# Kernel optimization log

Hardware: AMD Instinct MI355X
Metric: run time of the kernel (lower is better)

## Reference

```python
import jax, jax.numpy as jnp
import numpy as np

SIZE = 1024
N_HEAD = 16
HEAD_DIM = SIZE // N_HEAD


def setup_inputs() -> dict:
    key = jax.random.key(0)
    ks = jax.random.split(key, 5)
    s = 1.0 / np.sqrt(SIZE)
    return {
        "x": jax.random.normal(ks[0], (4, 2048, SIZE), dtype=jnp.float32),
        "w_qkv": jax.random.uniform(ks[1], (SIZE, 3 * SIZE), dtype=jnp.float32, minval=-s, maxval=s),
        "b_qkv": jax.random.uniform(ks[2], (3 * SIZE,), dtype=jnp.float32, minval=-s, maxval=s),
        "w_fc": jax.random.uniform(ks[3], (SIZE, SIZE), dtype=jnp.float32, minval=-s, maxval=s),
        "b_fc": jax.random.uniform(ks[4], (SIZE,), dtype=jnp.float32, minval=-s, maxval=s),
    }


def reference(x, w_qkv, b_qkv, w_fc, b_fc):
    B, S, D = x.shape
    qkv = x @ w_qkv + b_qkv                      # [B, S, 3D]
    qkv = qkv.reshape(B, S, 3, N_HEAD, HEAD_DIM)
    qkv = jnp.transpose(qkv, (2, 0, 3, 1, 4))    # [3, B, H, S, hd]
    q, k, v = qkv[0], qkv[1], qkv[2]
    scale = 1.0 / np.sqrt(HEAD_DIM).astype(np.float32)
    scores = jnp.einsum('bhqd,bhkd->bhqk', q, k) * scale
    attn = jax.nn.softmax(scores, axis=-1)
    out = jnp.einsum('bhqk,bhkd->bhqd', attn, v)  # [B, H, S, hd]
    out = jnp.transpose(out, (0, 2, 1, 3)).reshape(B, S, D)
    return out @ w_fc + b_fc
```

## Files before the change

kernel.cpp:

```cpp
#include <hip/hip_runtime.h>

#define DEV __device__ __forceinline__

typedef float  f32x4  __attribute__((ext_vector_type(4)));
typedef short  short8 __attribute__((ext_vector_type(8)));
typedef __bf16 bf16x8 __attribute__((ext_vector_type(8)));

DEV f32x4 mfma_bf16(short8 a, short8 b, f32x4 c) {
    return __builtin_amdgcn_mfma_f32_16x16x32_bf16(
        __builtin_bit_cast(bf16x8, a), __builtin_bit_cast(bf16x8, b), c, 0, 0, 0);
}

DEV void gload_lds16(const void* g, void* l) {
    __builtin_amdgcn_global_load_lds(
        (const __attribute__((address_space(1))) unsigned int*)g,
        (__attribute__((address_space(3))) unsigned int*)l, 16, 0, 0);
}

DEV short f2bf(float f) {
    return __builtin_bit_cast(short, (__bf16)f);
}

__global__ void cast_x(const float* __restrict__ in, unsigned short* __restrict__ out, int n) {
    int i = (blockIdx.x * 256 + threadIdx.x) * 8;
    if (i >= n) return;
    f32x4 a = *(const f32x4*)(in + i);
    f32x4 b = *(const f32x4*)(in + i + 4);
    short8 o;
    o[0] = f2bf(a[0]); o[1] = f2bf(a[1]); o[2] = f2bf(a[2]); o[3] = f2bf(a[3]);
    o[4] = f2bf(b[0]); o[5] = f2bf(b[1]); o[6] = f2bf(b[2]); o[7] = f2bf(b[3]);
    *(short8*)(out + i) = o;
}

__global__ void transpose_cast(const float* __restrict__ in, unsigned short* __restrict__ out,
                               int R, int C) {
    __shared__ float tile[64][65];
    int c0 = blockIdx.x * 64, r0 = blockIdx.y * 64;
    int tx = threadIdx.x & 63, ty = threadIdx.x >> 6;
#pragma unroll
    for (int i = 0; i < 16; i++) {
        int r = i * 4 + ty;
        tile[r][tx] = in[(size_t)(r0 + r) * C + c0 + tx];
    }
    __syncthreads();
#pragma unroll
    for (int i = 0; i < 16; i++) {
        int cc = i * 4 + ty;
        out[(size_t)(c0 + cc) * R + r0 + tx] = (unsigned short)f2bf(tile[tx][cc]);
    }
}

__global__ void transpose_v(const unsigned short* __restrict__ Vb,
                            unsigned short* __restrict__ Vt) {
    __shared__ __align__(16) unsigned short tile[64][72];
    const int t = threadIdx.x;
    const int s0 = blockIdx.x * 64;
    const size_t slab = (size_t)blockIdx.y * 2048 * 64;
#pragma unroll
    for (int i = 0; i < 2; i++) {
        int c = i * 256 + t;
        int s = c >> 3, ch = c & 7;
        short8 v = *(const short8*)(Vb + slab + (size_t)(s0 + s) * 64 + ch * 8);
        *(short8*)(&tile[s][ch * 8]) = v;
    }
    __syncthreads();
#pragma unroll
    for (int i = 0; i < 2; i++) {
        int c = i * 256 + t;
        int d = c & 63, sc = c >> 6;
        short8 o;
#pragma unroll
        for (int e = 0; e < 8; e++) o[e] = tile[sc * 8 + e][d];
        *(short8*)(Vt + slab + (size_t)d * 2048 + s0 + sc * 8) = o;
    }
}

template <int MODE>
__global__ __launch_bounds__(256, 2) void gemm_bt(
    const unsigned short* __restrict__ A, const unsigned short* __restrict__ Bt,
    const float* __restrict__ bias, float* __restrict__ out_f32,
    unsigned short* __restrict__ q_out, unsigned short* __restrict__ k_out,
    unsigned short* __restrict__ v_out, int K) {
    __shared__ __align__(16) char smem[32768];
    char* lA = smem;
    char* lB = smem + 16384;
    const int t = threadIdx.x;
    const int lane = t & 63, w = t >> 6;
    const int wr = w >> 1, wc = w & 1;
    const int rowBase = blockIdx.y * 128, colBase = blockIdx.x * 128;

    f32x4 acc[4][4] = {};

    for (int k0 = 0; k0 < K; k0 += 64) {
#pragma unroll
        for (int i = 0; i < 4; i++) {
            int c = i * 256 + t;
            int r = c >> 3, j = c & 7;
            int jj = j ^ (r & 7);
            gload_lds16(A  + (size_t)(rowBase + r) * K + k0 + jj * 8, lA + c * 16);
            gload_lds16(Bt + (size_t)(colBase + r) * K + k0 + jj * 8, lB + c * 16);
        }
        __syncthreads();
#pragma unroll
        for (int ks = 0; ks < 2; ks++) {
            const int colb = (ks * 4 + (lane >> 4)) * 16;
            short8 af[4], bfr[4];
#pragma unroll
            for (int m2 = 0; m2 < 4; m2++) {
                int r = wr * 64 + m2 * 16 + (lane & 15);
                af[m2] = *(const short8*)(lA + r * 128 + (colb ^ ((r & 7) << 4)));
            }
#pragma unroll
            for (int n2 = 0; n2 < 4; n2++) {
                int r = wc * 64 + n2 * 16 + (lane & 15);
                bfr[n2] = *(const short8*)(lB + r * 128 + (colb ^ ((r & 7) << 4)));
            }
#pragma unroll
            for (int m2 = 0; m2 < 4; m2++)
#pragma unroll
                for (int n2 = 0; n2 < 4; n2++)
                    acc[m2][n2] = mfma_bf16(af[m2], bfr[n2], acc[m2][n2]);
        }
        __syncthreads();
    }

#pragma unroll
    for (int n2 = 0; n2 < 4; n2++) {
        int gc = colBase + wc * 64 + n2 * 16 + (lane & 15);
        float bv = bias[gc];
#pragma unroll
        for (int m2 = 0; m2 < 4; m2++) {
            int grb = rowBase + wr * 64 + m2 * 16 + ((lane >> 4) << 2);
#pragma unroll
            for (int r2 = 0; r2 < 4; r2++) {
                int gr = grb + r2;
                float v = acc[m2][n2][r2] + bv;
                if (MODE == 0) {
                    int which = gc >> 10, rem = gc & 1023;
                    int h = rem >> 6, d = rem & 63;
                    int b = gr >> 11, s = gr & 2047;
                    size_t idx = ((size_t)((b * 16 + h) * 2048 + s)) * 64 + d;
                    unsigned short* dst = which == 0 ? q_out : (which == 1 ? k_out : v_out);
                    if (which == 0) v *= 0.18033688011112042f;
                    dst[idx] = (unsigned short)f2bf(v);
                } else {
                    out_f32[(size_t)gr * 1024 + gc] = v;
                }
            }
        }
    }
}

__global__ __launch_bounds__(256, 4) void fattn(
    const unsigned short* __restrict__ Qb, const unsigned short* __restrict__ Kb,
    const unsigned short* __restrict__ Vt, unsigned short* __restrict__ O) {
    __shared__ __align__(16) char smem[40960];
    const int t = threadIdx.x, lane = t & 63, w = t >> 6;
    const int g = lane >> 4, li = lane & 15;
    const int bh = blockIdx.y;
    const int q0 = blockIdx.x * 64;
    const size_t slab = (size_t)bh * 2048 * 64;
    char* lPw = smem + 32768 + w * 2048;

    short8 qf[2];
#pragma unroll
    for (int ks = 0; ks < 2; ks++)
        qf[ks] = *(const short8*)(Qb + slab + (size_t)(q0 + w * 16 + li) * 64 + ks * 32 + g * 8);

#define STAGE_KV(kv0, buf)                                                          \
    do {                                                                            \
        char* dK_ = smem + (buf) * 8192;                                            \
        char* dV_ = smem + 16384 + (buf) * 8192;                                    \
        _Pragma("unroll")                                                           \
        for (int i_ = 0; i_ < 2; i_++) {                                            \
            int c_ = i_ * 256 + t, r_ = c_ >> 3, j_ = c_ & 7, jj_ = j_ ^ (r_ & 7);  \
            gload_lds16(Kb + slab + (size_t)((kv0) + r_) * 64 + jj_ * 8,            \
                        dK_ + c_ * 16);                                             \
            gload_lds16(Vt + slab + (size_t)r_ * 2048 + (kv0) + jj_ * 8,            \
                        dV_ + c_ * 16);                                             \
        }                                                                           \
    } while (0)

    STAGE_KV(0, 0);

    float lsum[4] = {0.f, 0.f, 0.f, 0.f};
    f32x4 accO[4] = {};

    int cur = 0;
    for (int kt = 0; kt < 32; kt++) {
        __syncthreads();
        if (kt < 31) STAGE_KV((kt + 1) * 64, cur ^ 1);
        char* lKc = smem + cur * 8192;
        char* lVc = smem + 16384 + cur * 8192;

        f32x4 sfr[4] = {};
#pragma unroll
        for (int ks = 0; ks < 2; ks++) {
            const int colb = (ks * 4 + g) * 16;
#pragma unroll
            for (int n2 = 0; n2 < 4; n2++) {
                int kr = n2 * 16 + li;
                short8 bk = *(const short8*)(lKc + kr * 128 + (colb ^ ((kr & 7) << 4)));
                sfr[n2] = mfma_bf16(qf[ks], bk, sfr[n2]);
            }
        }

#pragma unroll
        for (int f = 0; f < 4; f++) {
            const int cb = (f * 16 + li) * 2;
#pragma unroll
            for (int j = 0; j < 4; j++) {
                float p = __builtin_amdgcn_exp2f(sfr[f][j]);
                lsum[j] += p;
                int pr = (g << 2) + j;
                *(short*)(lPw + pr * 128 + (cb ^ ((pr & 7) << 4))) = f2bf(p);
            }
        }

#pragma unroll
        for (int ks = 0; ks < 2; ks++) {
            const int colb = (ks * 4 + g) * 16;
            short8 ap = *(const short8*)(lPw + li * 128 + (colb ^ ((li & 7) << 4)));
#pragma unroll
            for (int n2 = 0; n2 < 4; n2++) {
                int dv = n2 * 16 + li;
                short8 bv = *(const short8*)(lVc + dv * 128 + (colb ^ ((dv & 7) << 4)));
                accO[n2] = mfma_bf16(ap, bv, accO[n2]);
            }
        }
        cur ^= 1;
    }
#undef STAGE_KV

#pragma unroll
    for (int j = 0; j < 4; j++) {
        float s = lsum[j];
        s += __shfl_xor(s, 1, 16);
        s += __shfl_xor(s, 2, 16);
        s += __shfl_xor(s, 4, 16);
        s += __shfl_xor(s, 8, 16);
        lsum[j] = s;
    }

    const int b = bh >> 4, h = bh & 15;
#pragma unroll
    for (int j = 0; j < 4; j++) {
        int qrow = q0 + w * 16 + (g << 2) + j;
        float inv = 1.f / lsum[j];
#pragma unroll
        for (int f = 0; f < 4; f++) {
            int d = f * 16 + li;
            O[((size_t)(b * 2048 + qrow)) * 1024 + h * 64 + d] =
                (unsigned short)f2bf(accO[f][j] * inv);
        }
    }
}

extern "C" void kernel_launch(void* const* d_in, const int* in_sizes, int n_in,
                              void* d_out, int out_size, void* d_ws, size_t ws_size,
                              hipStream_t stream) {
    const float* x     = (const float*)d_in[0];
    const float* w_qkv = (const float*)d_in[1];
    const float* b_qkv = (const float*)d_in[2];
    const float* w_fc  = (const float*)d_in[3];
    const float* b_fc  = (const float*)d_in[4];

    char* ws = (char*)d_ws;
    unsigned short* Xb    = (unsigned short*)(ws);
    unsigned short* WqkvT = (unsigned short*)(ws + 16777216);
    unsigned short* WfcT  = (unsigned short*)(ws + 23068672);
    unsigned short* Qb    = (unsigned short*)(ws + 25165824);
    unsigned short* Kb    = (unsigned short*)(ws + 41943040);
    unsigned short* Vb    = (unsigned short*)(ws + 58720256);
    unsigned short* Ao    = (unsigned short*)(ws + 75497472);
    unsigned short* Vt    = Xb;

    cast_x<<<dim3(8388608 / (256 * 8)), 256, 0, stream>>>(x, Xb, 8388608);
    transpose_cast<<<dim3(3072 / 64, 1024 / 64), 256, 0, stream>>>(w_qkv, WqkvT, 1024, 3072);
    transpose_cast<<<dim3(1024 / 64, 1024 / 64), 256, 0, stream>>>(w_fc, WfcT, 1024, 1024);

    gemm_bt<0><<<dim3(3072 / 128, 8192 / 128), 256, 0, stream>>>(
        Xb, WqkvT, b_qkv, nullptr, Qb, Kb, Vb, 1024);

    transpose_v<<<dim3(32, 64), 256, 0, stream>>>(Vb, Vt);

    fattn<<<dim3(32, 64), 256, 0, stream>>>(Qb, Kb, Vt, Ao);

    gemm_bt<1><<<dim3(1024 / 128, 8192 / 128), 256, 0, stream>>>(
        Ao, WfcT, b_fc, (float*)d_out, nullptr, nullptr, nullptr, 1024);
}
```

Baseline: 315.4 us.

## Rework flash attention with 32x32 MFMA and register-resident P via permlane swap

The attention kernel moves from 16x16x32 to 32x32x16 bf16 MFMA, computing S transposed (K as the A operand) so each wave handles 32 query rows and a block covers 128 queries. The softmax probabilities are packed to bf16 and rearranged into the PV A-operand layout with permlane32_swap instead of a round trip through LDS, which drops the per-wave P scratch. Each K/V tile is now reused across twice as many query rows, but the grid is halved, and the epilogue issues per-row shuffles and scalar stores.

```diff
diff --git a/kernel.cpp b/kernel.cpp
--- a/kernel.cpp
+++ b/kernel.cpp
@@ -2,12 +2,20 @@
 
 #define DEV __device__ __forceinline__
 
-typedef float  f32x4  __attribute__((ext_vector_type(4)));
-typedef short  short8 __attribute__((ext_vector_type(8)));
-typedef __bf16 bf16x8 __attribute__((ext_vector_type(8)));
+typedef float  f32x4   __attribute__((ext_vector_type(4)));
+typedef float  f32x16  __attribute__((ext_vector_type(16)));
+typedef short  short8  __attribute__((ext_vector_type(8)));
+typedef __bf16 bf16x8  __attribute__((ext_vector_type(8)));
+typedef unsigned u32x2 __attribute__((ext_vector_type(2)));
+typedef unsigned u32x4 __attribute__((ext_vector_type(4)));
 
 DEV f32x4 mfma_bf16(short8 a, short8 b, f32x4 c) {
     return __builtin_amdgcn_mfma_f32_16x16x32_bf16(
+        __builtin_bit_cast(bf16x8, a), __builtin_bit_cast(bf16x8, b), c, 0, 0, 0);
+}
+
+DEV f32x16 mfma32(short8 a, short8 b, f32x16 c) {
+    return __builtin_amdgcn_mfma_f32_32x32x16_bf16(
         __builtin_bit_cast(bf16x8, a), __builtin_bit_cast(bf16x8, b), c, 0, 0, 0);
 }
 
@@ -17,8 +25,16 @@
         (__attribute__((address_space(3))) unsigned int*)l, 16, 0, 0);
 }
 
-DEV short f2bf(float f) {
-    return __builtin_bit_cast(short, (__bf16)f);
+DEV short f2bf(float f) { return __builtin_bit_cast(short, (__bf16)f); }
+
+DEV unsigned pack_bf2(float lo, float hi) {
+    unsigned short a = __builtin_bit_cast(unsigned short, (__bf16)lo);
+    unsigned short b = __builtin_bit_cast(unsigned short, (__bf16)hi);
+    return ((unsigned)b << 16) | (unsigned)a;
+}
+
+DEV u32x2 pl32swap(unsigned a, unsigned b) {
+    return __builtin_amdgcn_permlane32_swap(a, b, false, false);
 }
 
 __global__ void cast_x(const float* __restrict__ in, unsigned short* __restrict__ out, int n) {
@@ -154,18 +170,17 @@
 __global__ __launch_bounds__(256, 4) void fattn(
     const unsigned short* __restrict__ Qb, const unsigned short* __restrict__ Kb,
     const unsigned short* __restrict__ Vt, unsigned short* __restrict__ O) {
-    __shared__ __align__(16) char smem[40960];
+    __shared__ __align__(16) char smem[32768];
     const int t = threadIdx.x, lane = t & 63, w = t >> 6;
-    const int g = lane >> 4, li = lane & 15;
+    const int h = lane >> 5, l5 = lane & 31;
     const int bh = blockIdx.y;
-    const int q0 = blockIdx.x * 64;
+    const int q0 = blockIdx.x * 128 + w * 32;
     const size_t slab = (size_t)bh * 2048 * 64;
-    char* lPw = smem + 32768 + w * 2048;
-
-    short8 qf[2];
-#pragma unroll
-    for (int ks = 0; ks < 2; ks++)
-        qf[ks] = *(const short8*)(Qb + slab + (size_t)(q0 + w * 16 + li) * 64 + ks * 32 + g * 8);
+
+    short8 qf[4];
+#pragma unroll
+    for (int s = 0; s < 4; s++)
+        qf[s] = *(const short8*)(Qb + slab + (size_t)(q0 + l5) * 64 + s * 16 + h * 8);
 
 #define STAGE_KV(kv0, buf)                                                          \
     do {                                                                            \
@@ -183,8 +198,8 @@
 
     STAGE_KV(0, 0);
 
-    float lsum[4] = {0.f, 0.f, 0.f, 0.f};
-    f32x4 accO[4] = {};
+    float lsum = 0.f;
+    f32x16 accO0 = {}, accO1 = {};
 
     int cur = 0;
     for (int kt = 0; kt < 32; kt++) {
@@ -193,66 +208,58 @@
         char* lKc = smem + cur * 8192;
         char* lVc = smem + 16384 + cur * 8192;
 
-        f32x4 sfr[4] = {};
-#pragma unroll
-        for (int ks = 0; ks < 2; ks++) {
-            const int colb = (ks * 4 + g) * 16;
-#pragma unroll
-            for (int n2 = 0; n2 < 4; n2++) {
-                int kr = n2 * 16 + li;
-                short8 bk = *(const short8*)(lKc + kr * 128 + (colb ^ ((kr & 7) << 4)));
-                sfr[n2] = mfma_bf16(qf[ks], bk, sfr[n2]);
-            }
-        }
-
-#pragma unroll
-        for (int f = 0; f < 4; f++) {
-            const int cb = (f * 16 + li) * 2;
-#pragma unroll
-            for (int j = 0; j < 4; j++) {
-                float p = __builtin_amdgcn_exp2f(sfr[f][j]);
-                lsum[j] += p;
-                int pr = (g << 2) + j;
-                *(short*)(lPw + pr * 128 + (cb ^ ((pr & 7) << 4))) = f2bf(p);
-            }
-        }
-
-#pragma unroll
-        for (int ks = 0; ks < 2; ks++) {
-            const int colb = (ks * 4 + g) * 16;
-            short8 ap = *(const short8*)(lPw + li * 128 + (colb ^ ((li & 7) << 4)));
-#pragma unroll
-            for (int n2 = 0; n2 < 4; n2++) {
-                int dv = n2 * 16 + li;
-                short8 bv = *(const short8*)(lVc + dv * 128 + (colb ^ ((dv & 7) << 4)));
-                accO[n2] = mfma_bf16(ap, bv, accO[n2]);
+        f32x16 st0 = {}, st1 = {};
+#pragma unroll
+        for (int s = 0; s < 4; s++) {
+            const int cb = s * 32 + h * 16;
+            short8 k0 = *(const short8*)(lKc + l5 * 128 + (cb ^ ((l5 & 7) << 4)));
+            short8 k1 = *(const short8*)(lKc + (32 + l5) * 128 + (cb ^ ((l5 & 7) << 4)));
+            st0 = mfma32(k0, qf[s], st0);
+            st1 = mfma32(k1, qf[s], st1);
+        }
+
+#pragma unroll
+        for (int kv2 = 0; kv2 < 2; kv2++) {
+            const f32x16 stc = kv2 ? st1 : st0;
+            unsigned pk[8];
+#pragma unroll
+            for (int i = 0; i < 8; i++) {
+                float p0 = __builtin_amdgcn_exp2f(stc[2 * i]);
+                float p1 = __builtin_amdgcn_exp2f(stc[2 * i + 1]);
+                lsum += p0 + p1;
+                pk[i] = pack_bf2(p0, p1);
+            }
+            u32x2 s02 = pl32swap(pk[0], pk[2]);
+            u32x2 s13 = pl32swap(pk[1], pk[3]);
+            u32x2 s46 = pl32swap(pk[4], pk[6]);
+            u32x2 s57 = pl32swap(pk[5], pk[7]);
+            u32x4 af0 = {s02[0], s13[0], s02[1], s13[1]};
+            u32x4 af1 = {s46[0], s57[0], s46[1], s57[1]};
+#pragma unroll
+            for (int s = 0; s < 2; s++) {
+                short8 ap = __builtin_bit_cast(short8, s == 0 ? af0 : af1);
+                const int cb = kv2 * 64 + s * 32 + h * 16;
+                short8 v0 = *(const short8*)(lVc + l5 * 128 + (cb ^ ((l5 & 7) << 4)));
+                short8 v1 = *(const short8*)(lVc + (32 + l5) * 128 + (cb ^ ((l5 & 7) << 4)));
+                accO0 = mfma32(ap, v0, accO0);
+                accO1 = mfma32(ap, v1, accO1);
             }
         }
         cur ^= 1;
     }
 #undef STAGE_KV
 
-#pragma unroll
-    for (int j = 0; j < 4; j++) {
-        float s = lsum[j];
-        s += __shfl_xor(s, 1, 16);
-        s += __shfl_xor(s, 2, 16);
-        s += __shfl_xor(s, 4, 16);
-        s += __shfl_xor(s, 8, 16);
-        lsum[j] = s;
-    }
-
-    const int b = bh >> 4, h = bh & 15;
-#pragma unroll
-    for (int j = 0; j < 4; j++) {
-        int qrow = q0 + w * 16 + (g << 2) + j;
-        float inv = 1.f / lsum[j];
-#pragma unroll
-        for (int f = 0; f < 4; f++) {
-            int d = f * 16 + li;
-            O[((size_t)(b * 2048 + qrow)) * 1024 + h * 64 + d] =
-                (unsigned short)f2bf(accO[f][j] * inv);
-        }
+    lsum += __shfl_xor(lsum, 32);
+    float inv = 1.f / lsum;
+
+    const int b = bh >> 4, hh = bh & 15;
+#pragma unroll
+    for (int r = 0; r < 16; r++) {
+        int row = (r & 3) + 8 * (r >> 2) + 4 * h;
+        float iv = __shfl(inv, row, 64);
+        size_t base = ((size_t)(b * 2048 + q0 + row)) * 1024 + hh * 64;
+        O[base + l5]      = (unsigned short)f2bf(accO0[r] * iv);
+        O[base + 32 + l5] = (unsigned short)f2bf(accO1[r] * iv);
     }
 }
 
@@ -284,7 +291,7 @@
 
     transpose_v<<<dim3(32, 64), 256, 0, stream>>>(Vb, Vt);
 
-    fattn<<<dim3(32, 64), 256, 0, stream>>>(Qb, Kb, Vt, Ao);
+    fattn<<<dim3(16, 64), 256, 0, stream>>>(Qb, Kb, Vt, Ao);
 
     gemm_bt<1><<<dim3(1024 / 128, 8192 / 128), 256, 0, stream>>>(
         Ao, WfcT, b_fc, (float*)d_out, nullptr, nullptr, nullptr, 1024);
```

New measurement: 276.8 us. 12.2% less time.
